# Performance work log

Hardware: AMD Instinct MI355X
Metric: run time of the kernel (lower is better)

Reference implementation:

```python
import jax, jax.numpy as jnp
import numpy as np


def setup_inputs() -> dict:
    key = jax.random.key(0)
    kq, kk, kv = jax.random.split(key, 3)
    B, S, H, D = 1, 4096, 16, 64
    q = jax.random.normal(kq, (B, S, H, D), dtype=jnp.float32)
    k = jax.random.normal(kk, (B, S, H, D), dtype=jnp.float32)
    v = jax.random.normal(kv, (B, S, H, D), dtype=jnp.float32)
    return {"q": q, "k": k, "v": v, "causal": 1}


def reference(q, k, v, causal):
    B, S, H, D = q.shape
    scale = D ** (-0.5)
    # scores: [B, H, S_q, S_k]
    scores = jnp.einsum("bqhd,bkhd->bhqk", q, k) * scale
    if causal:
        mask = jnp.triu(jnp.ones((S, S), dtype=bool), k=1)  # True above diagonal
        scores = jnp.where(mask, -jnp.inf, scores)
    attn = jax.nn.softmax(scores, axis=-1)
    out = jnp.einsum("bhqk,bkhd->bqhd", attn, v)
    return out
```

## Files before the change

### kernel.cpp

```cpp
#include <hip/hip_runtime.h>
#include <stdint.h>

#define S_LEN 4096
#define NH    16
#define HD    64
#define RSTR  (NH * HD)
#define LRSTR 18

typedef __attribute__((ext_vector_type(8))) __bf16 bf16x8;
typedef __attribute__((ext_vector_type(4))) short short4v;
typedef __attribute__((ext_vector_type(4))) float floatx4;

union BF4 { unsigned short u[4]; unsigned d[2]; short4v s; };

__device__ __forceinline__ unsigned pkbf(float a, float b) {
    unsigned ua = __builtin_bit_cast(unsigned, a) + 0x8000u;
    unsigned ub = __builtin_bit_cast(unsigned, b) + 0x8000u;
    return __builtin_amdgcn_perm(ub, ua, 0x07060302u);
}

__device__ __forceinline__ floatx4 mfma16(short4v a, short4v b, floatx4 c) {
#if __has_builtin(__builtin_amdgcn_mfma_f32_16x16x16bf16_1k)
    return __builtin_amdgcn_mfma_f32_16x16x16bf16_1k(a, b, c, 0, 0, 0);
#else
    floatx4 d;
    asm volatile("v_mfma_f32_16x16x16_bf16 %0, %1, %2, %3\n\ts_nop 7\n\ts_nop 7"
                 : "=v"(d) : "v"(a), "v"(b), "v"(c));
    return d;
#endif
}

__device__ __forceinline__ void gl16(const void* g, void* l) {
#if __has_builtin(__builtin_amdgcn_global_load_lds)
    __builtin_amdgcn_global_load_lds((const __attribute__((address_space(1))) unsigned int*)g,
                                     (__attribute__((address_space(3))) unsigned int*)l, 16, 0, 0);
#else
    *(uint4*)l = *(const uint4*)g;
#endif
}

__global__ __launch_bounds__(256)
void pp_kv(const float* __restrict__ K, const float* __restrict__ V,
           unsigned short* __restrict__ Kz, unsigned short* __restrict__ Vz) {
    __shared__ __align__(16) float vt[64][68];
    const int bid = blockIdx.x;
    const int h   = bid & 15;
    const int tau = bid >> 4;
    const int tid = threadIdx.x;
    {
        const int r = tid >> 2, gg = tid & 3;
        const float* kp = K + ((size_t)(64 * tau + r) * NH + h) * HD + 16 * gg;
        const float4 a = *reinterpret_cast<const float4*>(kp);
        const float4 b = *reinterpret_cast<const float4*>(kp + 4);
        const float4 c = *reinterpret_cast<const float4*>(kp + 8);
        const float4 d = *reinterpret_cast<const float4*>(kp + 12);
        uint4 f0, f1;
        f0.x = pkbf(a.x, a.y); f0.y = pkbf(a.z, a.w);
        f0.z = pkbf(b.x, b.y); f0.w = pkbf(b.z, b.w);
        f1.x = pkbf(c.x, c.y); f1.y = pkbf(c.z, c.w);
        f1.z = pkbf(d.x, d.y); f1.w = pkbf(d.z, d.w);
        unsigned short* out = Kz + ((size_t)(h * 64 + tau)) * 4096 + r * 64;
        *reinterpret_cast<uint4*>(out + (((2 * gg)     ^ (r & 7)) * 8)) = f0;
        *reinterpret_cast<uint4*>(out + (((2 * gg + 1) ^ (r & 7)) * 8)) = f1;
    }
    {
        const int r = tid >> 2, ch = tid & 3;
        const float* vrow = V + ((size_t)(64 * tau + r) * NH + h) * HD + 4 * ch;
        #pragma unroll
        for (int k2 = 0; k2 < 4; ++k2)
            *reinterpret_cast<float4*>(&vt[r][4 * ch + 16 * k2]) =
                *reinterpret_cast<const float4*>(vrow + 16 * k2);
    }
    __syncthreads();
    {
        const int dr = tid & 63, kg = tid >> 6;
        float x[16];
        #pragma unroll
        for (int j = 0; j < 16; ++j) x[j] = vt[16 * kg + j][dr];
        uint4 g0, g1;
        g0.x = pkbf(x[0],  x[1]);  g0.y = pkbf(x[2],  x[3]);
        g0.z = pkbf(x[4],  x[5]);  g0.w = pkbf(x[6],  x[7]);
        g1.x = pkbf(x[8],  x[9]);  g1.y = pkbf(x[10], x[11]);
        g1.z = pkbf(x[12], x[13]); g1.w = pkbf(x[14], x[15]);
        unsigned short* out = Vz + ((size_t)(h * 64 + tau)) * 4096 + dr * 64;
        *reinterpret_cast<uint4*>(out + (((2 * kg)     ^ (dr & 7)) * 8)) = g0;
        *reinterpret_cast<uint4*>(out + (((2 * kg + 1) ^ (dr & 7)) * 8)) = g1;
    }
}

__global__ __launch_bounds__(256, 3)
void fa_main(const float* __restrict__ Q, const unsigned short* __restrict__ Kz,
             const unsigned short* __restrict__ Vz, const int* __restrict__ causal_p,
             float* __restrict__ O) {
    __shared__ __align__(16) unsigned char smem[49152];
    unsigned short* Klds = (unsigned short*)smem;
    unsigned short* Vlds = (unsigned short*)(smem + 24576);
    unsigned short* Qlds = (unsigned short*)(smem + 16384);
    float* Lsum = (float*)smem;
    float* Lred = (float*)(smem + 16384);

    const int bid = blockIdx.x;
    const int h   = bid & 15;
    const int x   = 63 - (bid >> 4);
    const int q0  = x * 64;

    const int tid = threadIdx.x;
    const int wv  = tid >> 6;
    const int ln  = tid & 63;
    const int c16 = ln & 15;
    const int qd  = ln >> 4;
    const int causal = causal_p[0];

    const float SC = 0.18033688011112042f;

    const char* kg = (const char*)Kz + (size_t)h * 64 * 8192 + wv * 2048 + ln * 16;
    const char* vg = (const char*)Vz + (size_t)h * 64 * 8192 + wv * 2048 + ln * 16;
    char* kl = (char*)smem + wv * 2048 + ln * 16;
    char* vl = (char*)smem + 24576 + wv * 2048 + ln * 16;

#define GLDS_TILE(IT, BUF) do {                                  \
    const char* ks_ = kg + (size_t)(IT) * 8192;                  \
    const char* vs_ = vg + (size_t)(IT) * 8192;                  \
    char* kd_ = kl + (BUF) * 8192;                               \
    char* vd_ = vl + (BUF) * 8192;                               \
    gl16(ks_, kd_); gl16(ks_ + 1024, kd_ + 1024);                \
    gl16(vs_, vd_); gl16(vs_ + 1024, vd_ + 1024);                \
} while (0)

    GLDS_TILE(0, 0);
    GLDS_TILE(1, 1);

    {
        const int r = tid >> 2, gg = tid & 3;
        const float* qp = Q + ((size_t)(q0 + r) * NH + h) * HD + 16 * gg;
        const float4 a = *reinterpret_cast<const float4*>(qp);
        const float4 b = *reinterpret_cast<const float4*>(qp + 4);
        const float4 c = *reinterpret_cast<const float4*>(qp + 8);
        const float4 d = *reinterpret_cast<const float4*>(qp + 12);
        uint4 f0, f1;
        f0.x = pkbf(a.x * SC, a.y * SC); f0.y = pkbf(a.z * SC, a.w * SC);
        f0.z = pkbf(b.x * SC, b.y * SC); f0.w = pkbf(b.z * SC, b.w * SC);
        f1.x = pkbf(c.x * SC, c.y * SC); f1.y = pkbf(c.z * SC, c.w * SC);
        f1.z = pkbf(d.x * SC, d.y * SC); f1.w = pkbf(d.z * SC, d.w * SC);
        unsigned short* out = Qlds + r * 64;
        *reinterpret_cast<uint4*>(out + (((2 * gg)     ^ (r & 7)) * 8)) = f0;
        *reinterpret_cast<uint4*>(out + (((2 * gg + 1) ^ (r & 7)) * 8)) = f1;
    }

    const int nIter = causal ? (x + 1) : (S_LEN / 64);

    floatx4 acc[4][4];
    #pragma unroll
    for (int m = 0; m < 4; ++m)
        #pragma unroll
        for (int t = 0; t < 4; ++t) acc[m][t] = floatx4{0.f, 0.f, 0.f, 0.f};
    float lacc[4] = {0.f, 0.f, 0.f, 0.f};

    const int e7 = c16 & 7;
    const int o0 = (qd ^ e7) * 8;
    const int o1 = ((4 + qd) ^ e7) * 8;
    const int vo = ((2 * wv + (qd >> 1)) ^ e7) * 8 + (qd & 1) * 4;
    const int mlhs = 16 * wv + 4 * qd;

    const unsigned short* kb0 = Klds + (16 * wv + c16) * 64 + o0;
    const unsigned short* kb1 = Klds + (16 * wv + c16) * 64 + o1;
    const unsigned short* vb  = Vlds + c16 * 64 + vo;

    __syncthreads();

    bf16x8 qh0[4], qh1[4];
    #pragma unroll
    for (int t = 0; t < 4; ++t) {
        const unsigned short* qrow = Qlds + (16 * t + c16) * 64;
        qh0[t] = *reinterpret_cast<const bf16x8*>(qrow + o0);
        qh1[t] = *reinterpret_cast<const bf16x8*>(qrow + o1);
    }
    __syncthreads();

#define FA_BODY(IT, BUF, BUF2) do {                                          \
    if ((IT) == nIter - 1) { asm volatile("s_waitcnt vmcnt(0)" ::: "memory"); } \
    else                   { asm volatile("s_waitcnt vmcnt(4)" ::: "memory"); } \
    __builtin_amdgcn_s_barrier();                                            \
    if ((IT) + 2 < nIter) GLDS_TILE((IT) + 2, BUF2);                         \
    const bf16x8 kf0 = *reinterpret_cast<const bf16x8*>(kb0 + (BUF) * 4096); \
    const bf16x8 kf1 = *reinterpret_cast<const bf16x8*>(kb1 + (BUF) * 4096); \
    const bool maskit = (causal != 0) && ((IT) == nIter - 1);                \
    BF4 pf[4];                                                               \
    _Pragma("unroll")                                                        \
    for (int t = 0; t < 4; ++t) {                                            \
        floatx4 st = __builtin_amdgcn_mfma_f32_16x16x32_bf16(                \
            kf0, qh0[t], floatx4{0.f, 0.f, 0.f, 0.f}, 0, 0, 0);              \
        st = __builtin_amdgcn_mfma_f32_16x16x32_bf16(kf1, qh1[t], st, 0, 0, 0); \
        float p[4];                                                          \
        _Pragma("unroll")                                                    \
        for (int i = 0; i < 4; ++i) {                                        \
            float sv = st[i];                                                \
            if (maskit && (mlhs + i > 16 * t + c16)) sv = -1e30f;            \
            p[i] = __builtin_amdgcn_exp2f(sv);                               \
        }                                                                    \
        lacc[t] += (p[0] + p[1]) + (p[2] + p[3]);                            \
        pf[t].d[0] = pkbf(p[0], p[1]);                                       \
        pf[t].d[1] = pkbf(p[2], p[3]);                                       \
    }                                                                        \
    _Pragma("unroll")                                                        \
    for (int md = 0; md < 4; ++md) {                                         \
        BF4 vf;                                                              \
        *reinterpret_cast<uint2*>(&vf.d[0]) =                                \
            *reinterpret_cast<const uint2*>(vb + (BUF) * 4096 + md * 1024);  \
        _Pragma("unroll")                                                    \
        for (int t = 0; t < 4; ++t)                                          \
            acc[md][t] = mfma16(vf.s, pf[t].s, acc[md][t]);                  \
    }                                                                        \
} while (0)

    int it = 0;
    for (; it + 3 <= nIter; it += 3) {
        FA_BODY(it,     0, 2);
        FA_BODY(it + 1, 1, 0);
        FA_BODY(it + 2, 2, 1);
    }
    if (it < nIter)     FA_BODY(it,     0, 2);
    if (it + 1 < nIter) FA_BODY(it + 1, 1, 0);

    __syncthreads();

    #pragma unroll
    for (int t = 0; t < 4; ++t) {
        float lt = lacc[t];
        lt += __shfl_xor(lt, 16);
        lt += __shfl_xor(lt, 32);
        if (qd == 0) Lsum[wv * 64 + t * 16 + c16] = lt;
    }

    const int qi  = tid & 63;
    const int dg  = tid >> 6;
    const int lnr = 16 * dg + (qi & 15);
    const int jb  = 4 * (qi >> 4);
    float* orow = O + ((size_t)(q0 + qi) * NH + h) * HD;
    float inv = 0.f;

    for (int md = 0; md < 4; ++md) {
        float* Lw = Lred + (wv * 64 + ln) * LRSTR;
        #pragma unroll
        for (int t = 0; t < 4; ++t) {
            float2 w0; w0.x = acc[md][t][0]; w0.y = acc[md][t][1];
            float2 w1; w1.x = acc[md][t][2]; w1.y = acc[md][t][3];
            *reinterpret_cast<float2*>(&Lw[4 * t])     = w0;
            *reinterpret_cast<float2*>(&Lw[4 * t + 2]) = w1;
        }
        __syncthreads();
        if (md == 0) {
            const float l = Lsum[qi] + Lsum[64 + qi] + Lsum[128 + qi] + Lsum[192 + qi];
            inv = 1.0f / l;
        }
        float s0 = 0.f, s1 = 0.f, s2 = 0.f, s3 = 0.f;
        #pragma unroll
        for (int w = 0; w < 4; ++w) {
            const float* Lr = Lred + (w * 64 + lnr) * LRSTR + jb;
            s0 += Lr[0]; s1 += Lr[1]; s2 += Lr[2]; s3 += Lr[3];
        }
        floatx4 o; o[0] = s0 * inv; o[1] = s1 * inv; o[2] = s2 * inv; o[3] = s3 * inv;
        *reinterpret_cast<floatx4*>(orow + 16 * md + 4 * dg) = o;
        __syncthreads();
    }
}

extern "C" void kernel_launch(void* const* d_in, const int* in_sizes, int n_in,
                              void* d_out, int out_size, void* d_ws, size_t ws_size,
                              hipStream_t stream) {
    const float* q = (const float*)d_in[0];
    const float* k = (const float*)d_in[1];
    const float* v = (const float*)d_in[2];
    const int* causal = (const int*)d_in[3];
    float* out = (float*)d_out;
    unsigned short* Kz = (unsigned short*)d_ws;
    unsigned short* Vz = Kz + (size_t)NH * 64 * 4096;
    pp_kv<<<dim3(64 * NH), dim3(256), 0, stream>>>(k, v, Kz, Vz);
    fa_main<<<dim3(64 * NH), dim3(256), 0, stream>>>(q, Kz, Vz, causal, out);
}
```

Measured before the change: 168.0 us.

## Restructure K/V pipeline into double-buffered two-tile stages with priority boost

Replaces the triple-buffered per-tile K/V async load loop with a double-buffered scheme in which each stage holds two 64-row tiles, so one barrier and a full vmcnt(0) wait cover two tiles of compute. LDS grows to 64KB and the occupancy hint drops from 3 to 2 blocks per CU. MFMA work is wrapped in s_setprio(1) to favour compute waves. The aim is to halve barrier and wait overhead per tile, at the cost of fewer resident blocks and a less fine-grained prefetch overlap.

```diff
diff --git a/kernel.cpp b/kernel.cpp
--- a/kernel.cpp
+++ b/kernel.cpp
@@ -88,13 +88,11 @@
     }
 }
 
-__global__ __launch_bounds__(256, 3)
+__global__ __launch_bounds__(256, 2)
 void fa_main(const float* __restrict__ Q, const unsigned short* __restrict__ Kz,
              const unsigned short* __restrict__ Vz, const int* __restrict__ causal_p,
              float* __restrict__ O) {
-    __shared__ __align__(16) unsigned char smem[49152];
-    unsigned short* Klds = (unsigned short*)smem;
-    unsigned short* Vlds = (unsigned short*)(smem + 24576);
+    __shared__ __align__(16) unsigned char smem[65536];
     unsigned short* Qlds = (unsigned short*)(smem + 16384);
     float* Lsum = (float*)smem;
     float* Lred = (float*)(smem + 16384);
@@ -116,19 +114,22 @@
     const char* kg = (const char*)Kz + (size_t)h * 64 * 8192 + wv * 2048 + ln * 16;
     const char* vg = (const char*)Vz + (size_t)h * 64 * 8192 + wv * 2048 + ln * 16;
     char* kl = (char*)smem + wv * 2048 + ln * 16;
-    char* vl = (char*)smem + 24576 + wv * 2048 + ln * 16;
-
-#define GLDS_TILE(IT, BUF) do {                                  \
+    char* vl = (char*)smem + 32768 + wv * 2048 + ln * 16;
+
+#define GS_TILE(IT, SB, T) do {                                  \
     const char* ks_ = kg + (size_t)(IT) * 8192;                  \
     const char* vs_ = vg + (size_t)(IT) * 8192;                  \
-    char* kd_ = kl + (BUF) * 8192;                               \
-    char* vd_ = vl + (BUF) * 8192;                               \
+    char* kd_ = kl + (SB) * 16384 + (T) * 8192;                  \
+    char* vd_ = vl + (SB) * 16384 + (T) * 8192;                  \
     gl16(ks_, kd_); gl16(ks_ + 1024, kd_ + 1024);                \
     gl16(vs_, vd_); gl16(vs_ + 1024, vd_ + 1024);                \
 } while (0)
 
-    GLDS_TILE(0, 0);
-    GLDS_TILE(1, 1);
+    const int nIter = causal ? (x + 1) : (S_LEN / 64);
+    const int nS    = (nIter + 1) >> 1;
+
+    GS_TILE(0, 0, 0);
+    if (nIter > 1) GS_TILE(1, 0, 1);
 
     {
         const int r = tid >> 2, gg = tid & 3;
@@ -147,8 +148,6 @@
         *reinterpret_cast<uint4*>(out + (((2 * gg + 1) ^ (r & 7)) * 8)) = f1;
     }
 
-    const int nIter = causal ? (x + 1) : (S_LEN / 64);
-
     floatx4 acc[4][4];
     #pragma unroll
     for (int m = 0; m < 4; ++m)
@@ -161,10 +160,6 @@
     const int o1 = ((4 + qd) ^ e7) * 8;
     const int vo = ((2 * wv + (qd >> 1)) ^ e7) * 8 + (qd & 1) * 4;
     const int mlhs = 16 * wv + 4 * qd;
-
-    const unsigned short* kb0 = Klds + (16 * wv + c16) * 64 + o0;
-    const unsigned short* kb1 = Klds + (16 * wv + c16) * 64 + o1;
-    const unsigned short* vb  = Vlds + c16 * 64 + vo;
 
     __syncthreads();
 
@@ -177,13 +172,12 @@
     }
     __syncthreads();
 
-#define FA_BODY(IT, BUF, BUF2) do {                                          \
-    if ((IT) == nIter - 1) { asm volatile("s_waitcnt vmcnt(0)" ::: "memory"); } \
-    else                   { asm volatile("s_waitcnt vmcnt(4)" ::: "memory"); } \
-    __builtin_amdgcn_s_barrier();                                            \
-    if ((IT) + 2 < nIter) GLDS_TILE((IT) + 2, BUF2);                         \
-    const bf16x8 kf0 = *reinterpret_cast<const bf16x8*>(kb0 + (BUF) * 4096); \
-    const bf16x8 kf1 = *reinterpret_cast<const bf16x8*>(kb1 + (BUF) * 4096); \
+#define FA_TILE(IT, SB, T) do {                                              \
+    const unsigned short* Kb = (const unsigned short*)(smem + (SB) * 16384 + (T) * 8192); \
+    const unsigned short* Vb = (const unsigned short*)(smem + 32768 + (SB) * 16384 + (T) * 8192); \
+    const unsigned short* krow = Kb + (16 * wv + c16) * 64;                  \
+    const bf16x8 kf0 = *reinterpret_cast<const bf16x8*>(krow + o0);          \
+    const bf16x8 kf1 = *reinterpret_cast<const bf16x8*>(krow + o1);          \
     const bool maskit = (causal != 0) && ((IT) == nIter - 1);                \
     BF4 pf[4];                                                               \
     _Pragma("unroll")                                                        \
@@ -205,22 +199,29 @@
     _Pragma("unroll")                                                        \
     for (int md = 0; md < 4; ++md) {                                         \
         BF4 vf;                                                              \
-        *reinterpret_cast<uint2*>(&vf.d[0]) =                                \
-            *reinterpret_cast<const uint2*>(vb + (BUF) * 4096 + md * 1024);  \
+        const unsigned short* vrow = Vb + (16 * md + c16) * 64 + vo;         \
+        *reinterpret_cast<uint2*>(&vf.d[0]) = *reinterpret_cast<const uint2*>(vrow); \
         _Pragma("unroll")                                                    \
         for (int t = 0; t < 4; ++t)                                          \
             acc[md][t] = mfma16(vf.s, pf[t].s, acc[md][t]);                  \
     }                                                                        \
 } while (0)
 
-    int it = 0;
-    for (; it + 3 <= nIter; it += 3) {
-        FA_BODY(it,     0, 2);
-        FA_BODY(it + 1, 1, 0);
-        FA_BODY(it + 2, 2, 1);
-    }
-    if (it < nIter)     FA_BODY(it,     0, 2);
-    if (it + 1 < nIter) FA_BODY(it + 1, 1, 0);
+    for (int s = 0; s < nS; ++s) {
+        const int sb = s & 1;
+        asm volatile("s_waitcnt vmcnt(0)" ::: "memory");
+        __builtin_amdgcn_s_barrier();
+
+        if (s + 1 < nS) {
+            GS_TILE(2 * s + 2, sb ^ 1, 0);
+            if (2 * s + 3 < nIter) GS_TILE(2 * s + 3, sb ^ 1, 1);
+        }
+
+        __builtin_amdgcn_s_setprio(1);
+        FA_TILE(2 * s, sb, 0);
+        if (2 * s + 1 < nIter) FA_TILE(2 * s + 1, sb, 1);
+        __builtin_amdgcn_s_setprio(0);
+    }
 
     __syncthreads();
 
```

Result: faster. 150.1 us (-10.6%).
